# Kernel tuning notes

Measured on AMD Instinct MI355X. Metric: run time of the kernel, lower is better.

The kernel has to match this reference:

```python
import math
import jax, jax.numpy as jnp
import numpy as np

B, T, C, H = 2, 2048, 1024, 16

def setup_inputs() -> dict:
    key = jax.random.key(0)
    k1, k2, k3 = jax.random.split(key, 3)
    x = jax.random.normal(k1, (B, T, C), dtype=jnp.float32)
    W_kqv = jax.random.normal(k2, (C, 3 * C), dtype=jnp.float32) * (1.0 / math.sqrt(C))
    W_proj = jax.random.normal(k3, (C, C), dtype=jnp.float32) * (1.0 / math.sqrt(C))
    b_proj = jnp.zeros((C,), dtype=jnp.float32)
    return {"x": x, "W_kqv": W_kqv, "W_proj": W_proj, "b_proj": b_proj}

def reference(x, W_kqv, W_proj, b_proj):
    Bx, Tx, Cx = x.shape
    hs = Cx // H  # head size
    q, k, v = jnp.split(x @ W_kqv, 3, axis=2)  # each (B,T,C)
    # (B,T,C) -> (B,H,T,hs)
    q = q.reshape(Bx, Tx, H, hs).transpose(0, 2, 1, 3)
    k = k.reshape(Bx, Tx, H, hs).transpose(0, 2, 1, 3)
    v = v.reshape(Bx, Tx, H, hs).transpose(0, 2, 1, 3)
    attn = jnp.einsum('bhqd,bhkd->bhqk', q, k) / math.sqrt(hs)  # (B,H,T,T)
    causal = jnp.tril(jnp.ones((Tx, Tx), dtype=bool))
    attn = jnp.where(causal, attn, -jnp.inf)
    attn = jax.nn.softmax(attn, axis=-1)
    y = jnp.einsum('bhqk,bhkd->bhqd', attn, v)  # (B,H,T,hs)
    y = y.transpose(0, 2, 1, 3).reshape(Bx, Tx, Cx)
    return y @ W_proj + b_proj
```

## Files before the change

### kernel.cpp

```cpp
#include <hip/hip_runtime.h>


typedef unsigned short u16;
typedef unsigned int u32;
typedef __bf16 bf16x8 __attribute__((ext_vector_type(8)));
typedef float f32x4 __attribute__((ext_vector_type(4)));
typedef u32 u32x4 __attribute__((ext_vector_type(4)));
typedef u16 u16x4 __attribute__((ext_vector_type(4)));

__device__ __forceinline__ u16 f2bf(float f) {
  u32 u = __float_as_uint(f);
  u32 r = u + 0x7FFFu + ((u >> 16) & 1u);
  return (u16)(r >> 16);
}

__device__ __forceinline__ bf16x8 ld_bf8(const u16* p) {
  union { u32x4 u; bf16x8 b; } x;
  x.u = *(const u32x4*)p;
  return x.b;
}

__device__ __forceinline__ void gld_lds16(const u16* g, u16* l) {
  __builtin_amdgcn_global_load_lds(
      (const __attribute__((address_space(1))) u32*)g,
      (__attribute__((address_space(3))) u32*)l, 16, 0, 0);
}

__global__ __launch_bounds__(256) void conv_x_kernel(const float* __restrict__ src,
                                                     u16* __restrict__ dst) {
  int idx = blockIdx.x * 256 + threadIdx.x;
  const float4* s4 = (const float4*)src;
  float4 a = s4[2 * idx], b = s4[2 * idx + 1];
  union { u16 h[8]; u32x4 v; } pk;
  pk.h[0] = f2bf(a.x); pk.h[1] = f2bf(a.y); pk.h[2] = f2bf(a.z); pk.h[3] = f2bf(a.w);
  pk.h[4] = f2bf(b.x); pk.h[5] = f2bf(b.y); pk.h[6] = f2bf(b.z); pk.h[7] = f2bf(b.w);
  *(u32x4*)&dst[(size_t)idx * 8] = pk.v;
}

__global__ __launch_bounds__(256) void convT_kernel(const float* __restrict__ src,
                                                    u16* __restrict__ dst, int R, int Cc) {
  __shared__ float ls[64][65];
  int r0 = blockIdx.x * 64, c0 = blockIdx.y * 64;
  int t = threadIdx.x;
  for (int u = t; u < 1024; u += 256) {
    int r = u >> 4, cs = (u & 15) << 2;
    float4 v = *(const float4*)&src[(size_t)(r0 + r) * Cc + (c0 + cs)];
    ls[r][cs] = v.x; ls[r][cs + 1] = v.y; ls[r][cs + 2] = v.z; ls[r][cs + 3] = v.w;
  }
  __syncthreads();
  for (int u = t; u < 1024; u += 256) {
    int n = u >> 4, ks = (u & 15) << 2;
    u16x4 o;
    o.x = f2bf(ls[ks][n]); o.y = f2bf(ls[ks + 1][n]);
    o.z = f2bf(ls[ks + 2][n]); o.w = f2bf(ls[ks + 3][n]);
    *(u16x4*)&dst[(size_t)(c0 + n) * R + (r0 + ks)] = o;
  }
}

__global__ __launch_bounds__(256) void qkv_gemm_kernel(
    const u16* __restrict__ A, const u16* __restrict__ Bt,
    u16* __restrict__ Qh, u16* __restrict__ Kh, u16* __restrict__ Vh, float qscale) {
  constexpr int K = 1024;
  __shared__ __align__(16) u16 As[128 * 32];
  __shared__ __align__(16) u16 Bs[128 * 32];
  int t = threadIdx.x;
  int wave = t >> 6, lane = t & 63, quad = lane >> 4, l16 = lane & 15;
  int wm = (wave >> 1) << 6, wn = (wave & 1) << 6;
  int m0 = blockIdx.x * 128, n0 = blockIdx.y * 128;
  f32x4 acc[4][4] = {};
  int u0 = t, u1 = t + 256;
  int ra0 = u0 >> 2, ca0 = ((u0 & 3) ^ ((u0 >> 3) & 3)) << 3;
  int ra1 = u1 >> 2, ca1 = ((u1 & 3) ^ ((u1 >> 3) & 3)) << 3;
  int swq = (quad ^ ((l16 >> 1) & 3)) << 3;
  for (int k0 = 0; k0 < K; k0 += 32) {
    gld_lds16(&A[(size_t)(m0 + ra0) * K + k0 + ca0], &As[u0 * 8]);
    gld_lds16(&A[(size_t)(m0 + ra1) * K + k0 + ca1], &As[u1 * 8]);
    gld_lds16(&Bt[(size_t)(n0 + ra0) * K + k0 + ca0], &Bs[u0 * 8]);
    gld_lds16(&Bt[(size_t)(n0 + ra1) * K + k0 + ca1], &Bs[u1 * 8]);
    __syncthreads();
    bf16x8 af[4], bfr[4];
    for (int r = 0; r < 4; ++r) af[r] = ld_bf8(&As[(wm + r * 16 + l16) * 32 + swq]);
    for (int c = 0; c < 4; ++c) bfr[c] = ld_bf8(&Bs[(wn + c * 16 + l16) * 32 + swq]);
    for (int r = 0; r < 4; ++r)
      for (int c = 0; c < 4; ++c)
        acc[r][c] = __builtin_amdgcn_mfma_f32_16x16x32_bf16(af[r], bfr[c], acc[r][c], 0, 0, 0);
    __syncthreads();
  }
  for (int r = 0; r < 4; ++r) {
    int rowbase = m0 + wm + r * 16 + quad * 4;
    for (int c = 0; c < 4; ++c) {
      int col = n0 + wn + c * 16 + l16;
      int seg = col >> 10;
      int cc = col & 1023;
      int h = cc >> 6, d = cc & 63;
      for (int i = 0; i < 4; ++i) {
        int row = rowbase + i;
        int b = row >> 11, tt = row & 2047;
        size_t off = (((size_t)(b * 16 + h)) * 2048 + tt) * 64 + d;
        float v = acc[r][c][i];
        if (seg == 0)      Qh[off] = f2bf(v * qscale);
        else if (seg == 1) Kh[off] = f2bf(v);
        else               Vh[off] = f2bf(v);
      }
    }
  }
}

__global__ __launch_bounds__(256) void vT_kernel(const u16* __restrict__ Vh,
                                                 u16* __restrict__ Vt) {
  __shared__ __align__(16) u16 ls[64 * 72];
  int t = threadIdx.x;
  int t0 = blockIdx.x * 64, bh = blockIdx.y;
  const u16* in = Vh + ((size_t)bh * 2048 + t0) * 64;
  for (int u = t; u < 512; u += 256) {
    int row = u >> 3, col = (u & 7) << 3;
    *(u32x4*)&ls[row * 72 + col] = *(const u32x4*)&in[(size_t)row * 64 + col];
  }
  __syncthreads();
  for (int u = t; u < 512; u += 256) {
    int d = u >> 3, tc = (u & 7) << 3;
    union { u16 h[8]; u32x4 v; } pk;
    for (int j = 0; j < 8; ++j) pk.h[j] = ls[(tc + j) * 72 + d];
    *(u32x4*)&Vt[((size_t)bh * 64 + d) * 2048 + t0 + tc] = pk.v;
  }
}

__global__ __launch_bounds__(512) void proj_gemm_kernel(
    const u16* __restrict__ A, const u16* __restrict__ Bt,
    float* __restrict__ out, const float* __restrict__ bias) {
  constexpr int K = 1024;
  __shared__ __align__(16) u16 As[128 * 32];
  __shared__ __align__(16) u16 Bs[128 * 32];
  int t = threadIdx.x;
  int wave = t >> 6, lane = t & 63, quad = lane >> 4, l16 = lane & 15;
  int wm = (wave >> 2) << 6, wn = (wave & 3) << 5;
  int m0 = blockIdx.x * 128, n0 = blockIdx.y * 128;
  f32x4 acc[4][2] = {};
  int u0 = t;
  int ra0 = u0 >> 2, ca0 = ((u0 & 3) ^ ((u0 >> 3) & 3)) << 3;
  int swq = (quad ^ ((l16 >> 1) & 3)) << 3;
  for (int k0 = 0; k0 < K; k0 += 32) {
    gld_lds16(&A[(size_t)(m0 + ra0) * K + k0 + ca0], &As[u0 * 8]);
    gld_lds16(&Bt[(size_t)(n0 + ra0) * K + k0 + ca0], &Bs[u0 * 8]);
    __syncthreads();
    bf16x8 af[4], bfr[2];
    for (int r = 0; r < 4; ++r) af[r] = ld_bf8(&As[(wm + r * 16 + l16) * 32 + swq]);
    for (int c = 0; c < 2; ++c) bfr[c] = ld_bf8(&Bs[(wn + c * 16 + l16) * 32 + swq]);
    for (int r = 0; r < 4; ++r)
      for (int c = 0; c < 2; ++c)
        acc[r][c] = __builtin_amdgcn_mfma_f32_16x16x32_bf16(af[r], bfr[c], acc[r][c], 0, 0, 0);
    __syncthreads();
  }
  for (int r = 0; r < 4; ++r) {
    int rowbase = m0 + wm + r * 16 + quad * 4;
    for (int c = 0; c < 2; ++c) {
      int col = n0 + wn + c * 16 + l16;
      float bv = bias[col];
      for (int i = 0; i < 4; ++i)
        out[(size_t)(rowbase + i) * 1024 + col] = acc[r][c][i] + bv;
    }
  }
}

__global__ __launch_bounds__(256, 6) void flash_kernel(
    const u16* __restrict__ Qh, const u16* __restrict__ Kh, const u16* __restrict__ Vt,
    u16* __restrict__ yb, float* __restrict__ Opart) {
  __shared__ __align__(16) u16 Ks[64 * 64];
  __shared__ __align__(16) u16 Vs[64 * 64];
  __shared__ __align__(16) u16 Ps[64 * 64];
  int t = threadIdx.x, wave = t >> 6, lane = t & 63, quad = lane >> 4, l16 = lane & 15;
  int id = blockIdx.x;
  int g = id / 360, r = id % 360;
  int bh = g * 8 + (r & 7);
  int jx = r >> 3;
  int qtile, kvs, kve, sidx = 0, half = 0;
  bool partial;
  if (jx < 19) {
    qtile = 18 - jx; kvs = 0; kve = qtile + 1; partial = false;
  } else {
    sidx = (jx - 19) >> 1; half = (jx - 19) & 1;
    qtile = 31 - sidx;
    int nkv = qtile + 1, mid = nkv >> 1;
    kvs = half ? mid : 0; kve = half ? nkv : mid; partial = true;
  }
  int q0 = qtile << 6;
  const u16* Qb = Qh + (size_t)bh * 2048 * 64;
  const u16* Kb = Kh + (size_t)bh * 2048 * 64;
  const u16* Vb = Vt + (size_t)bh * 64 * 2048;
  bf16x8 qa0, qa1;
  {
    int qrow = q0 + wave * 16 + l16;
    qa0 = ld_bf8(&Qb[(size_t)qrow * 64 + quad * 8]);
    qa1 = ld_bf8(&Qb[(size_t)qrow * 64 + 32 + quad * 8]);
  }
  f32x4 oacc[4] = {};
  float lsum = 0.f;
  int u0 = wave * 128 + lane, u1 = u0 + 64;
  int r0 = u0 >> 3, p0 = u0 & 7, cb0 = (p0 - r0) & 7;
  int r1s = u1 >> 3, p1 = u1 & 7, cb1 = (p1 - r1s) & 7;
  for (int j = kvs; j < kve; ++j) {
    int kv0 = j << 6;
    __syncthreads();
    gld_lds16(&Kb[(size_t)(kv0 + r0) * 64 + cb0 * 8], &Ks[u0 * 8]);
    gld_lds16(&Kb[(size_t)(kv0 + r1s) * 64 + cb1 * 8], &Ks[u1 * 8]);
    gld_lds16(&Vb[(size_t)r0 * 2048 + kv0 + cb0 * 8], &Vs[u0 * 8]);
    gld_lds16(&Vb[(size_t)r1s * 2048 + kv0 + cb1 * 8], &Vs[u1 * 8]);
    __syncthreads();
    bool maskit = (j == qtile);
    for (int c = 0; c < 4; ++c) {
      int krow = c * 16 + l16;
      bf16x8 kb0 = ld_bf8(&Ks[krow * 64 + ((quad + krow) & 7) * 8]);
      bf16x8 kb1 = ld_bf8(&Ks[krow * 64 + ((quad + 4 + krow) & 7) * 8]);
      f32x4 z = {0.f, 0.f, 0.f, 0.f};
      z = __builtin_amdgcn_mfma_f32_16x16x32_bf16(kb0, qa0, z, 0, 0, 0);
      z = __builtin_amdgcn_mfma_f32_16x16x32_bf16(kb1, qa1, z, 0, 0, 0);
      int prow = wave * 16 + l16;
      union { u16 hh[4]; u16x4 v; } pk;
      for (int i = 0; i < 4; ++i) {
        float p = __builtin_amdgcn_exp2f(z[i]);
        if (maskit && (kv0 + c * 16 + quad * 4 + i > q0 + wave * 16 + l16)) p = 0.f;
        lsum += p;
        pk.hh[i] = f2bf(p);
      }
      *(u16x4*)&Ps[prow * 64 + ((2 * c + (quad >> 1) + prow) & 7) * 8 + (quad & 1) * 4] = pk.v;
    }
    int prow = wave * 16 + l16;
    bf16x8 pa0 = ld_bf8(&Ps[prow * 64 + ((quad + prow) & 7) * 8]);
    bf16x8 pa1 = ld_bf8(&Ps[prow * 64 + ((quad + 4 + prow) & 7) * 8]);
    for (int dt = 0; dt < 4; ++dt) {
      int vrow = dt * 16 + l16;
      bf16x8 vb0 = ld_bf8(&Vs[vrow * 64 + ((quad + vrow) & 7) * 8]);
      bf16x8 vb1 = ld_bf8(&Vs[vrow * 64 + ((quad + 4 + vrow) & 7) * 8]);
      oacc[dt] = __builtin_amdgcn_mfma_f32_16x16x32_bf16(pa0, vb0, oacc[dt], 0, 0, 0);
      oacc[dt] = __builtin_amdgcn_mfma_f32_16x16x32_bf16(pa1, vb1, oacc[dt], 0, 0, 0);
    }
  }
  lsum += __shfl_xor(lsum, 16);
  lsum += __shfl_xor(lsum, 32);
  if (partial) {
    float* Op = Opart + ((size_t)(bh * 13 + sidx) * 2 + half) * 4160;
    for (int dt = 0; dt < 4; ++dt)
      for (int i = 0; i < 4; ++i)
        Op[(wave * 16 + quad * 4 + i) * 64 + dt * 16 + l16] = oacc[dt][i];
    if (quad == 0) Op[4096 + wave * 16 + l16] = lsum;
  } else {
    int b = bh >> 4, h = bh & 15;
    for (int i = 0; i < 4; ++i) {
      float inv = 1.0f / __shfl(lsum, quad * 4 + i);
      int qq = q0 + wave * 16 + quad * 4 + i;
      size_t rowoff = ((size_t)(b * 2048 + qq)) * 1024 + h * 64;
      for (int dt = 0; dt < 4; ++dt)
        yb[rowoff + dt * 16 + l16] = f2bf(oacc[dt][i] * inv);
    }
  }
}

__global__ __launch_bounds__(256) void combine_kernel(const float* __restrict__ Opart,
                                                      u16* __restrict__ yb) {
  int sidx = blockIdx.x, bh = blockIdx.y, t = threadIdx.x;
  int qtile = 31 - sidx;
  const float* A = Opart + (size_t)(bh * 13 + sidx) * 2 * 4160;
  const float* Bp = A + 4160;
  int q = t >> 2, d0 = (t & 3) << 4;
  float inv = 1.0f / (A[4096 + q] + Bp[4096 + q]);
  int b = bh >> 4, h = bh & 15;
  size_t off = ((size_t)(b * 2048 + (qtile << 6) + q)) * 1024 + h * 64 + d0;
  union { u16 hh[16]; u32x4 v[2]; } pk;
  for (int k = 0; k < 16; ++k)
    pk.hh[k] = f2bf((A[q * 64 + d0 + k] + Bp[q * 64 + d0 + k]) * inv);
  *(u32x4*)&yb[off] = pk.v[0];
  *(u32x4*)&yb[off + 8] = pk.v[1];
}

extern "C" void kernel_launch(void* const* d_in, const int* in_sizes, int n_in,
                              void* d_out, int out_size, void* d_ws, size_t ws_size,
                              hipStream_t stream) {
  const float* x     = (const float*)d_in[0];
  const float* Wkqv  = (const float*)d_in[1];
  const float* Wproj = (const float*)d_in[2];
  const float* bproj = (const float*)d_in[3];
  float* out = (float*)d_out;

  u16* ws     = (u16*)d_ws;
  u16* xb     = ws;
  u16* wkqvT  = xb + (size_t)4096 * 1024;
  u16* wprojT = wkqvT + (size_t)3072 * 1024;
  u16* Qh     = wprojT + (size_t)1024 * 1024;
  u16* Kh     = Qh + (size_t)32 * 2048 * 64;
  u16* Vt     = Kh + (size_t)32 * 2048 * 64;
  u16* yb     = Vt + (size_t)32 * 2048 * 64;
  u16* Vh     = yb;
  float* Opart = (float*)ws;

  const float QSCALE = 0.18033688011112042f;

  conv_x_kernel<<<2048, 256, 0, stream>>>(x, xb);
  convT_kernel<<<dim3(16, 48), 256, 0, stream>>>(Wkqv, wkqvT, 1024, 3072);
  convT_kernel<<<dim3(16, 16), 256, 0, stream>>>(Wproj, wprojT, 1024, 1024);
  qkv_gemm_kernel<<<dim3(32, 24), 256, 0, stream>>>(xb, wkqvT, Qh, Kh, Vh, QSCALE);
  vT_kernel<<<dim3(32, 32), 256, 0, stream>>>(Vh, Vt);
  flash_kernel<<<1440, 256, 0, stream>>>(Qh, Kh, Vt, yb, Opart);
  combine_kernel<<<dim3(13, 32), 256, 0, stream>>>(Opart, yb);
  proj_gemm_kernel<<<dim3(32, 8), 512, 0, stream>>>(yb, wprojT, out, bproj);
}
```

Measured before the change: 189.3 us.

## Fuse prep kernels, write V transposed from QKV GEMM, widen flash waves

```diff
diff --git a/kernel.cpp b/kernel.cpp
--- a/kernel.cpp
+++ b/kernel.cpp
@@ -26,43 +26,56 @@
       (__attribute__((address_space(3))) u32*)l, 16, 0, 0);
 }
 
-__global__ __launch_bounds__(256) void conv_x_kernel(const float* __restrict__ src,
-                                                     u16* __restrict__ dst) {
-  int idx = blockIdx.x * 256 + threadIdx.x;
-  const float4* s4 = (const float4*)src;
-  float4 a = s4[2 * idx], b = s4[2 * idx + 1];
-  union { u16 h[8]; u32x4 v; } pk;
-  pk.h[0] = f2bf(a.x); pk.h[1] = f2bf(a.y); pk.h[2] = f2bf(a.z); pk.h[3] = f2bf(a.w);
-  pk.h[4] = f2bf(b.x); pk.h[5] = f2bf(b.y); pk.h[6] = f2bf(b.z); pk.h[7] = f2bf(b.w);
-  *(u32x4*)&dst[(size_t)idx * 8] = pk.v;
-}
-
-__global__ __launch_bounds__(256) void convT_kernel(const float* __restrict__ src,
-                                                    u16* __restrict__ dst, int R, int Cc) {
-  __shared__ float ls[64][65];
-  int r0 = blockIdx.x * 64, c0 = blockIdx.y * 64;
+__device__ __forceinline__ void convT_body(const float* __restrict__ src,
+                                           u16* __restrict__ dst, int R, int Cc,
+                                           int r0, int c0, float* ls ) {
   int t = threadIdx.x;
   for (int u = t; u < 1024; u += 256) {
     int r = u >> 4, cs = (u & 15) << 2;
     float4 v = *(const float4*)&src[(size_t)(r0 + r) * Cc + (c0 + cs)];
-    ls[r][cs] = v.x; ls[r][cs + 1] = v.y; ls[r][cs + 2] = v.z; ls[r][cs + 3] = v.w;
+    ls[r * 65 + cs] = v.x; ls[r * 65 + cs + 1] = v.y;
+    ls[r * 65 + cs + 2] = v.z; ls[r * 65 + cs + 3] = v.w;
   }
   __syncthreads();
   for (int u = t; u < 1024; u += 256) {
     int n = u >> 4, ks = (u & 15) << 2;
     u16x4 o;
-    o.x = f2bf(ls[ks][n]); o.y = f2bf(ls[ks + 1][n]);
-    o.z = f2bf(ls[ks + 2][n]); o.w = f2bf(ls[ks + 3][n]);
+    o.x = f2bf(ls[ks * 65 + n]); o.y = f2bf(ls[(ks + 1) * 65 + n]);
+    o.z = f2bf(ls[(ks + 2) * 65 + n]); o.w = f2bf(ls[(ks + 3) * 65 + n]);
     *(u16x4*)&dst[(size_t)(c0 + n) * R + (r0 + ks)] = o;
+  }
+}
+
+__global__ __launch_bounds__(256) void prep_kernel(
+    const float* __restrict__ x, const float* __restrict__ Wkqv,
+    const float* __restrict__ Wproj, u16* __restrict__ xb,
+    u16* __restrict__ wkqvT, u16* __restrict__ wprojT) {
+  __shared__ float ls[64 * 65];
+  int bx = blockIdx.x;
+  if (bx < 2048) {
+    int idx = bx * 256 + threadIdx.x;
+    const float4* s4 = (const float4*)x;
+    float4 a = s4[2 * idx], b = s4[2 * idx + 1];
+    union { u16 h[8]; u32x4 v; } pk;
+    pk.h[0] = f2bf(a.x); pk.h[1] = f2bf(a.y); pk.h[2] = f2bf(a.z); pk.h[3] = f2bf(a.w);
+    pk.h[4] = f2bf(b.x); pk.h[5] = f2bf(b.y); pk.h[6] = f2bf(b.z); pk.h[7] = f2bf(b.w);
+    *(u32x4*)&xb[(size_t)idx * 8] = pk.v;
+  } else if (bx < 2816) {
+    int idx = bx - 2048;
+    convT_body(Wkqv, wkqvT, 1024, 3072, (idx & 15) * 64, (idx >> 4) * 64, ls);
+  } else {
+    int idx = bx - 2816;
+    convT_body(Wproj, wprojT, 1024, 1024, (idx & 15) * 64, (idx >> 4) * 64, ls);
   }
 }
 
 __global__ __launch_bounds__(256) void qkv_gemm_kernel(
     const u16* __restrict__ A, const u16* __restrict__ Bt,
-    u16* __restrict__ Qh, u16* __restrict__ Kh, u16* __restrict__ Vh, float qscale) {
+    u16* __restrict__ Qh, u16* __restrict__ Kh, u16* __restrict__ Vt, float qscale) {
   constexpr int K = 1024;
-  __shared__ __align__(16) u16 As[128 * 32];
-  __shared__ __align__(16) u16 Bs[128 * 32];
+  __shared__ __align__(16) u16 smem[8704];
+  u16* As = smem;
+  u16* Bs = smem + 4096;
   int t = threadIdx.x;
   int wave = t >> 6, lane = t & 63, quad = lane >> 4, l16 = lane & 15;
   int wm = (wave >> 1) << 6, wn = (wave & 1) << 6;
@@ -86,42 +99,48 @@
         acc[r][c] = __builtin_amdgcn_mfma_f32_16x16x32_bf16(af[r], bfr[c], acc[r][c], 0, 0, 0);
     __syncthreads();
   }
-  for (int r = 0; r < 4; ++r) {
-    int rowbase = m0 + wm + r * 16 + quad * 4;
-    for (int c = 0; c < 4; ++c) {
-      int col = n0 + wn + c * 16 + l16;
-      int seg = col >> 10;
-      int cc = col & 1023;
-      int h = cc >> 6, d = cc & 63;
-      for (int i = 0; i < 4; ++i) {
-        int row = rowbase + i;
-        int b = row >> 11, tt = row & 2047;
-        size_t off = (((size_t)(b * 16 + h)) * 2048 + tt) * 64 + d;
-        float v = acc[r][c][i];
-        if (seg == 0)      Qh[off] = f2bf(v * qscale);
-        else if (seg == 1) Kh[off] = f2bf(v);
-        else               Vh[off] = f2bf(v);
-      }
-    }
-  }
-}
-
-__global__ __launch_bounds__(256) void vT_kernel(const u16* __restrict__ Vh,
-                                                 u16* __restrict__ Vt) {
-  __shared__ __align__(16) u16 ls[64 * 72];
-  int t = threadIdx.x;
-  int t0 = blockIdx.x * 64, bh = blockIdx.y;
-  const u16* in = Vh + ((size_t)bh * 2048 + t0) * 64;
-  for (int u = t; u < 512; u += 256) {
-    int row = u >> 3, col = (u & 7) << 3;
-    *(u32x4*)&ls[row * 72 + col] = *(const u32x4*)&in[(size_t)row * 64 + col];
-  }
-  __syncthreads();
-  for (int u = t; u < 512; u += 256) {
-    int d = u >> 3, tc = (u & 7) << 3;
-    union { u16 h[8]; u32x4 v; } pk;
-    for (int j = 0; j < 8; ++j) pk.h[j] = ls[(tc + j) * 72 + d];
-    *(u32x4*)&Vt[((size_t)bh * 64 + d) * 2048 + t0 + tc] = pk.v;
+  if (n0 < 2048) {
+    for (int r = 0; r < 4; ++r) {
+      int rowbase = m0 + wm + r * 16 + quad * 4;
+      for (int c = 0; c < 4; ++c) {
+        int col = n0 + wn + c * 16 + l16;
+        int seg = col >> 10;
+        int cc = col & 1023;
+        int h = cc >> 6, d = cc & 63;
+        for (int i = 0; i < 4; ++i) {
+          int row = rowbase + i;
+          int b = row >> 11, tt = row & 2047;
+          size_t off = (((size_t)(b * 16 + h)) * 2048 + tt) * 64 + d;
+          float v = acc[r][c][i];
+          if (seg == 0) Qh[off] = f2bf(v * qscale);
+          else          Kh[off] = f2bf(v);
+        }
+      }
+    }
+  } else {
+    int h0 = (n0 - 2048) >> 6;
+    int b = m0 >> 11, tt0 = m0 & 2047;
+    for (int p = 0; p < 2; ++p) {
+      __syncthreads();
+      if (wn == p * 64) {
+        for (int r = 0; r < 4; ++r) {
+          int row = wm + r * 16 + quad * 4;
+          for (int c = 0; c < 4; ++c) {
+            int col = c * 16 + l16;
+            union { u16 hh[4]; u16x4 v; } pk;
+            for (int i = 0; i < 4; ++i) pk.hh[i] = f2bf(acc[r][c][i]);
+            *(u16x4*)&smem[col * 136 + row] = pk.v;
+          }
+        }
+      }
+      __syncthreads();
+      int bh = b * 16 + h0 + p;
+      for (int w = t; w < 1024; w += 256) {
+        int col = w >> 4, ch = w & 15;
+        u32x4 v = *(u32x4*)&smem[col * 136 + ch * 8];
+        *(u32x4*)&Vt[((size_t)bh * 64 + col) * 2048 + tt0 + ch * 8] = v;
+      }
+    }
   }
 }
 
@@ -162,7 +181,7 @@
   }
 }
 
-__global__ __launch_bounds__(256, 6) void flash_kernel(
+__global__ __launch_bounds__(128, 3) void flash_kernel(
     const u16* __restrict__ Qh, const u16* __restrict__ Kh, const u16* __restrict__ Vt,
     u16* __restrict__ yb, float* __restrict__ Opart) {
   __shared__ __align__(16) u16 Ks[64 * 64];
@@ -187,71 +206,92 @@
   const u16* Qb = Qh + (size_t)bh * 2048 * 64;
   const u16* Kb = Kh + (size_t)bh * 2048 * 64;
   const u16* Vb = Vt + (size_t)bh * 64 * 2048;
-  bf16x8 qa0, qa1;
-  {
-    int qrow = q0 + wave * 16 + l16;
-    qa0 = ld_bf8(&Qb[(size_t)qrow * 64 + quad * 8]);
-    qa1 = ld_bf8(&Qb[(size_t)qrow * 64 + 32 + quad * 8]);
-  }
-  f32x4 oacc[4] = {};
-  float lsum = 0.f;
-  int u0 = wave * 128 + lane, u1 = u0 + 64;
-  int r0 = u0 >> 3, p0 = u0 & 7, cb0 = (p0 - r0) & 7;
-  int r1s = u1 >> 3, p1 = u1 & 7, cb1 = (p1 - r1s) & 7;
+  bf16x8 qa[2][2];
+  for (int s = 0; s < 2; ++s) {
+    int qrow = q0 + wave * 32 + s * 16 + l16;
+    qa[s][0] = ld_bf8(&Qb[(size_t)qrow * 64 + quad * 8]);
+    qa[s][1] = ld_bf8(&Qb[(size_t)qrow * 64 + 32 + quad * 8]);
+  }
+  f32x4 oacc[2][4] = {};
+  float lsum[2] = {0.f, 0.f};
   for (int j = kvs; j < kve; ++j) {
     int kv0 = j << 6;
     __syncthreads();
-    gld_lds16(&Kb[(size_t)(kv0 + r0) * 64 + cb0 * 8], &Ks[u0 * 8]);
-    gld_lds16(&Kb[(size_t)(kv0 + r1s) * 64 + cb1 * 8], &Ks[u1 * 8]);
-    gld_lds16(&Vb[(size_t)r0 * 2048 + kv0 + cb0 * 8], &Vs[u0 * 8]);
-    gld_lds16(&Vb[(size_t)r1s * 2048 + kv0 + cb1 * 8], &Vs[u1 * 8]);
+    for (int k = 0; k < 4; ++k) {
+      int u = wave * 256 + k * 64 + lane;
+      int row = u >> 3, cb = ((u & 7) - row) & 7;
+      gld_lds16(&Kb[(size_t)(kv0 + row) * 64 + cb * 8], &Ks[u * 8]);
+      gld_lds16(&Vb[(size_t)row * 2048 + kv0 + cb * 8], &Vs[u * 8]);
+    }
     __syncthreads();
     bool maskit = (j == qtile);
     for (int c = 0; c < 4; ++c) {
       int krow = c * 16 + l16;
       bf16x8 kb0 = ld_bf8(&Ks[krow * 64 + ((quad + krow) & 7) * 8]);
       bf16x8 kb1 = ld_bf8(&Ks[krow * 64 + ((quad + 4 + krow) & 7) * 8]);
-      f32x4 z = {0.f, 0.f, 0.f, 0.f};
-      z = __builtin_amdgcn_mfma_f32_16x16x32_bf16(kb0, qa0, z, 0, 0, 0);
-      z = __builtin_amdgcn_mfma_f32_16x16x32_bf16(kb1, qa1, z, 0, 0, 0);
-      int prow = wave * 16 + l16;
-      union { u16 hh[4]; u16x4 v; } pk;
-      for (int i = 0; i < 4; ++i) {
-        float p = __builtin_amdgcn_exp2f(z[i]);
-        if (maskit && (kv0 + c * 16 + quad * 4 + i > q0 + wave * 16 + l16)) p = 0.f;
-        lsum += p;
-        pk.hh[i] = f2bf(p);
-      }
-      *(u16x4*)&Ps[prow * 64 + ((2 * c + (quad >> 1) + prow) & 7) * 8 + (quad & 1) * 4] = pk.v;
-    }
-    int prow = wave * 16 + l16;
-    bf16x8 pa0 = ld_bf8(&Ps[prow * 64 + ((quad + prow) & 7) * 8]);
-    bf16x8 pa1 = ld_bf8(&Ps[prow * 64 + ((quad + 4 + prow) & 7) * 8]);
+      for (int s = 0; s < 2; ++s) {
+        f32x4 z = {0.f, 0.f, 0.f, 0.f};
+        z = __builtin_amdgcn_mfma_f32_16x16x32_bf16(kb0, qa[s][0], z, 0, 0, 0);
+        z = __builtin_amdgcn_mfma_f32_16x16x32_bf16(kb1, qa[s][1], z, 0, 0, 0);
+        int prow = wave * 32 + s * 16 + l16;
+        union { u16 hh[4]; u16x4 v; } pk;
+        if (maskit) {
+          int qg = q0 + prow;
+          for (int i = 0; i < 4; ++i) {
+            float p = __builtin_amdgcn_exp2f(z[i]);
+            if (kv0 + c * 16 + quad * 4 + i > qg) p = 0.f;
+            lsum[s] += p;
+            pk.hh[i] = f2bf(p);
+          }
+        } else {
+          for (int i = 0; i < 4; ++i) {
+            float p = __builtin_amdgcn_exp2f(z[i]);
+            lsum[s] += p;
+            pk.hh[i] = f2bf(p);
+          }
+        }
+        *(u16x4*)&Ps[prow * 64 + ((2 * c + (quad >> 1) + prow) & 7) * 8 + (quad & 1) * 4] =
+            pk.v;
+      }
+    }
+    bf16x8 pa[2][2];
+    for (int s = 0; s < 2; ++s) {
+      int prow = wave * 32 + s * 16 + l16;
+      pa[s][0] = ld_bf8(&Ps[prow * 64 + ((quad + prow) & 7) * 8]);
+      pa[s][1] = ld_bf8(&Ps[prow * 64 + ((quad + 4 + prow) & 7) * 8]);
+    }
     for (int dt = 0; dt < 4; ++dt) {
       int vrow = dt * 16 + l16;
       bf16x8 vb0 = ld_bf8(&Vs[vrow * 64 + ((quad + vrow) & 7) * 8]);
       bf16x8 vb1 = ld_bf8(&Vs[vrow * 64 + ((quad + 4 + vrow) & 7) * 8]);
-      oacc[dt] = __builtin_amdgcn_mfma_f32_16x16x32_bf16(pa0, vb0, oacc[dt], 0, 0, 0);
-      oacc[dt] = __builtin_amdgcn_mfma_f32_16x16x32_bf16(pa1, vb1, oacc[dt], 0, 0, 0);
-    }
-  }
-  lsum += __shfl_xor(lsum, 16);
-  lsum += __shfl_xor(lsum, 32);
+      for (int s = 0; s < 2; ++s) {
+        oacc[s][dt] = __builtin_amdgcn_mfma_f32_16x16x32_bf16(pa[s][0], vb0, oacc[s][dt], 0, 0, 0);
+        oacc[s][dt] = __builtin_amdgcn_mfma_f32_16x16x32_bf16(pa[s][1], vb1, oacc[s][dt], 0, 0, 0);
+      }
+    }
+  }
+  for (int s = 0; s < 2; ++s) {
+    lsum[s] += __shfl_xor(lsum[s], 16);
+    lsum[s] += __shfl_xor(lsum[s], 32);
+  }
   if (partial) {
     float* Op = Opart + ((size_t)(bh * 13 + sidx) * 2 + half) * 4160;
-    for (int dt = 0; dt < 4; ++dt)
-      for (int i = 0; i < 4; ++i)
-        Op[(wave * 16 + quad * 4 + i) * 64 + dt * 16 + l16] = oacc[dt][i];
-    if (quad == 0) Op[4096 + wave * 16 + l16] = lsum;
+    for (int s = 0; s < 2; ++s) {
+      for (int dt = 0; dt < 4; ++dt)
+        for (int i = 0; i < 4; ++i)
+          Op[(wave * 32 + s * 16 + quad * 4 + i) * 64 + dt * 16 + l16] = oacc[s][dt][i];
+      if (quad == 0) Op[4096 + wave * 32 + s * 16 + l16] = lsum[s];
+    }
   } else {
     int b = bh >> 4, h = bh & 15;
-    for (int i = 0; i < 4; ++i) {
-      float inv = 1.0f / __shfl(lsum, quad * 4 + i);
-      int qq = q0 + wave * 16 + quad * 4 + i;
-      size_t rowoff = ((size_t)(b * 2048 + qq)) * 1024 + h * 64;
-      for (int dt = 0; dt < 4; ++dt)
-        yb[rowoff + dt * 16 + l16] = f2bf(oacc[dt][i] * inv);
-    }
+    for (int s = 0; s < 2; ++s)
+      for (int i = 0; i < 4; ++i) {
+        float inv = 1.0f / __shfl(lsum[s], quad * 4 + i);
+        int qq = q0 + wave * 32 + s * 16 + quad * 4 + i;
+        size_t rowoff = ((size_t)(b * 2048 + qq)) * 1024 + h * 64;
+        for (int dt = 0; dt < 4; ++dt)
+          yb[rowoff + dt * 16 + l16] = f2bf(oacc[s][dt][i] * inv);
+      }
   }
 }
 
@@ -289,17 +329,13 @@
   u16* Kh     = Qh + (size_t)32 * 2048 * 64;
   u16* Vt     = Kh + (size_t)32 * 2048 * 64;
   u16* yb     = Vt + (size_t)32 * 2048 * 64;
-  u16* Vh     = yb;
   float* Opart = (float*)ws;
 
   const float QSCALE = 0.18033688011112042f;
 
-  conv_x_kernel<<<2048, 256, 0, stream>>>(x, xb);
-  convT_kernel<<<dim3(16, 48), 256, 0, stream>>>(Wkqv, wkqvT, 1024, 3072);
-  convT_kernel<<<dim3(16, 16), 256, 0, stream>>>(Wproj, wprojT, 1024, 1024);
-  qkv_gemm_kernel<<<dim3(32, 24), 256, 0, stream>>>(xb, wkqvT, Qh, Kh, Vh, QSCALE);
-  vT_kernel<<<dim3(32, 32), 256, 0, stream>>>(Vh, Vt);
-  flash_kernel<<<1440, 256, 0, stream>>>(Qh, Kh, Vt, yb, Opart);
+  prep_kernel<<<3072, 256, 0, stream>>>(x, Wkqv, Wproj, xb, wkqvT, wprojT);
+  qkv_gemm_kernel<<<dim3(32, 24), 256, 0, stream>>>(xb, wkqvT, Qh, Kh, Vt, QSCALE);
+  flash_kernel<<<1440, 128, 0, stream>>>(Qh, Kh, Vt, yb, Opart);
   combine_kernel<<<dim3(13, 32), 256, 0, stream>>>(Opart, yb);
   proj_gemm_kernel<<<dim3(32, 8), 512, 0, stream>>>(yb, wprojT, out, bproj);
 }
```

After: 205.0 us. +8.3%, slower.

## Fuse prep conversions into one launch, retile proj GEMM, split masked softmax path

Applied to the files above, without the earlier changes.

```diff
diff --git a/kernel.cpp b/kernel.cpp
--- a/kernel.cpp
+++ b/kernel.cpp
@@ -26,34 +26,46 @@
       (__attribute__((address_space(3))) u32*)l, 16, 0, 0);
 }
 
-__global__ __launch_bounds__(256) void conv_x_kernel(const float* __restrict__ src,
-                                                     u16* __restrict__ dst) {
-  int idx = blockIdx.x * 256 + threadIdx.x;
-  const float4* s4 = (const float4*)src;
-  float4 a = s4[2 * idx], b = s4[2 * idx + 1];
-  union { u16 h[8]; u32x4 v; } pk;
-  pk.h[0] = f2bf(a.x); pk.h[1] = f2bf(a.y); pk.h[2] = f2bf(a.z); pk.h[3] = f2bf(a.w);
-  pk.h[4] = f2bf(b.x); pk.h[5] = f2bf(b.y); pk.h[6] = f2bf(b.z); pk.h[7] = f2bf(b.w);
-  *(u32x4*)&dst[(size_t)idx * 8] = pk.v;
-}
-
-__global__ __launch_bounds__(256) void convT_kernel(const float* __restrict__ src,
-                                                    u16* __restrict__ dst, int R, int Cc) {
-  __shared__ float ls[64][65];
-  int r0 = blockIdx.x * 64, c0 = blockIdx.y * 64;
+__device__ __forceinline__ void convT_body(const float* __restrict__ src,
+                                           u16* __restrict__ dst, int R, int Cc,
+                                           int r0, int c0, float* ls ) {
   int t = threadIdx.x;
   for (int u = t; u < 1024; u += 256) {
     int r = u >> 4, cs = (u & 15) << 2;
     float4 v = *(const float4*)&src[(size_t)(r0 + r) * Cc + (c0 + cs)];
-    ls[r][cs] = v.x; ls[r][cs + 1] = v.y; ls[r][cs + 2] = v.z; ls[r][cs + 3] = v.w;
+    ls[r * 65 + cs] = v.x; ls[r * 65 + cs + 1] = v.y;
+    ls[r * 65 + cs + 2] = v.z; ls[r * 65 + cs + 3] = v.w;
   }
   __syncthreads();
   for (int u = t; u < 1024; u += 256) {
     int n = u >> 4, ks = (u & 15) << 2;
     u16x4 o;
-    o.x = f2bf(ls[ks][n]); o.y = f2bf(ls[ks + 1][n]);
-    o.z = f2bf(ls[ks + 2][n]); o.w = f2bf(ls[ks + 3][n]);
+    o.x = f2bf(ls[ks * 65 + n]); o.y = f2bf(ls[(ks + 1) * 65 + n]);
+    o.z = f2bf(ls[(ks + 2) * 65 + n]); o.w = f2bf(ls[(ks + 3) * 65 + n]);
     *(u16x4*)&dst[(size_t)(c0 + n) * R + (r0 + ks)] = o;
+  }
+}
+
+__global__ __launch_bounds__(256) void prep_kernel(
+    const float* __restrict__ x, const float* __restrict__ Wkqv,
+    const float* __restrict__ Wproj, u16* __restrict__ xb,
+    u16* __restrict__ wkqvT, u16* __restrict__ wprojT) {
+  __shared__ float ls[64 * 65];
+  int bx = blockIdx.x;
+  if (bx < 2048) {
+    int idx = bx * 256 + threadIdx.x;
+    const float4* s4 = (const float4*)x;
+    float4 a = s4[2 * idx], b = s4[2 * idx + 1];
+    union { u16 h[8]; u32x4 v; } pk;
+    pk.h[0] = f2bf(a.x); pk.h[1] = f2bf(a.y); pk.h[2] = f2bf(a.z); pk.h[3] = f2bf(a.w);
+    pk.h[4] = f2bf(b.x); pk.h[5] = f2bf(b.y); pk.h[6] = f2bf(b.z); pk.h[7] = f2bf(b.w);
+    *(u32x4*)&xb[(size_t)idx * 8] = pk.v;
+  } else if (bx < 2816) {
+    int idx = bx - 2048;
+    convT_body(Wkqv, wkqvT, 1024, 3072, (idx & 15) * 64, (idx >> 4) * 64, ls);
+  } else {
+    int idx = bx - 2816;
+    convT_body(Wproj, wprojT, 1024, 1024, (idx & 15) * 64, (idx >> 4) * 64, ls);
   }
 }
 
@@ -125,17 +137,17 @@
   }
 }
 
-__global__ __launch_bounds__(512) void proj_gemm_kernel(
+__global__ __launch_bounds__(256) void proj_gemm_kernel(
     const u16* __restrict__ A, const u16* __restrict__ Bt,
     float* __restrict__ out, const float* __restrict__ bias) {
   constexpr int K = 1024;
-  __shared__ __align__(16) u16 As[128 * 32];
-  __shared__ __align__(16) u16 Bs[128 * 32];
+  __shared__ __align__(16) u16 As[64 * 32];
+  __shared__ __align__(16) u16 Bs[64 * 32];
   int t = threadIdx.x;
   int wave = t >> 6, lane = t & 63, quad = lane >> 4, l16 = lane & 15;
-  int wm = (wave >> 2) << 6, wn = (wave & 3) << 5;
-  int m0 = blockIdx.x * 128, n0 = blockIdx.y * 128;
-  f32x4 acc[4][2] = {};
+  int wm = (wave >> 1) << 5, wn = (wave & 1) << 5;
+  int m0 = blockIdx.x * 64, n0 = blockIdx.y * 64;
+  f32x4 acc[2][2] = {};
   int u0 = t;
   int ra0 = u0 >> 2, ca0 = ((u0 & 3) ^ ((u0 >> 3) & 3)) << 3;
   int swq = (quad ^ ((l16 >> 1) & 3)) << 3;
@@ -143,15 +155,15 @@
     gld_lds16(&A[(size_t)(m0 + ra0) * K + k0 + ca0], &As[u0 * 8]);
     gld_lds16(&Bt[(size_t)(n0 + ra0) * K + k0 + ca0], &Bs[u0 * 8]);
     __syncthreads();
-    bf16x8 af[4], bfr[2];
-    for (int r = 0; r < 4; ++r) af[r] = ld_bf8(&As[(wm + r * 16 + l16) * 32 + swq]);
+    bf16x8 af[2], bfr[2];
+    for (int r = 0; r < 2; ++r) af[r] = ld_bf8(&As[(wm + r * 16 + l16) * 32 + swq]);
     for (int c = 0; c < 2; ++c) bfr[c] = ld_bf8(&Bs[(wn + c * 16 + l16) * 32 + swq]);
-    for (int r = 0; r < 4; ++r)
+    for (int r = 0; r < 2; ++r)
       for (int c = 0; c < 2; ++c)
         acc[r][c] = __builtin_amdgcn_mfma_f32_16x16x32_bf16(af[r], bfr[c], acc[r][c], 0, 0, 0);
     __syncthreads();
   }
-  for (int r = 0; r < 4; ++r) {
+  for (int r = 0; r < 2; ++r) {
     int rowbase = m0 + wm + r * 16 + quad * 4;
     for (int c = 0; c < 2; ++c) {
       int col = n0 + wn + c * 16 + l16;
@@ -216,11 +228,20 @@
       z = __builtin_amdgcn_mfma_f32_16x16x32_bf16(kb1, qa1, z, 0, 0, 0);
       int prow = wave * 16 + l16;
       union { u16 hh[4]; u16x4 v; } pk;
-      for (int i = 0; i < 4; ++i) {
-        float p = __builtin_amdgcn_exp2f(z[i]);
-        if (maskit && (kv0 + c * 16 + quad * 4 + i > q0 + wave * 16 + l16)) p = 0.f;
-        lsum += p;
-        pk.hh[i] = f2bf(p);
+      if (maskit) {
+        int qg = q0 + prow;
+        for (int i = 0; i < 4; ++i) {
+          float p = __builtin_amdgcn_exp2f(z[i]);
+          if (kv0 + c * 16 + quad * 4 + i > qg) p = 0.f;
+          lsum += p;
+          pk.hh[i] = f2bf(p);
+        }
+      } else {
+        for (int i = 0; i < 4; ++i) {
+          float p = __builtin_amdgcn_exp2f(z[i]);
+          lsum += p;
+          pk.hh[i] = f2bf(p);
+        }
       }
       *(u16x4*)&Ps[prow * 64 + ((2 * c + (quad >> 1) + prow) & 7) * 8 + (quad & 1) * 4] = pk.v;
     }
@@ -294,12 +315,10 @@
 
   const float QSCALE = 0.18033688011112042f;
 
-  conv_x_kernel<<<2048, 256, 0, stream>>>(x, xb);
-  convT_kernel<<<dim3(16, 48), 256, 0, stream>>>(Wkqv, wkqvT, 1024, 3072);
-  convT_kernel<<<dim3(16, 16), 256, 0, stream>>>(Wproj, wprojT, 1024, 1024);
+  prep_kernel<<<3072, 256, 0, stream>>>(x, Wkqv, Wproj, xb, wkqvT, wprojT);
   qkv_gemm_kernel<<<dim3(32, 24), 256, 0, stream>>>(xb, wkqvT, Qh, Kh, Vh, QSCALE);
   vT_kernel<<<dim3(32, 32), 256, 0, stream>>>(Vh, Vt);
   flash_kernel<<<1440, 256, 0, stream>>>(Qh, Kh, Vt, yb, Opart);
   combine_kernel<<<dim3(13, 32), 256, 0, stream>>>(Opart, yb);
-  proj_gemm_kernel<<<dim3(32, 8), 512, 0, stream>>>(yb, wprojT, out, bproj);
-}
+  proj_gemm_kernel<<<dim3(64, 16), 256, 0, stream>>>(yb, wprojT, out, bproj);
+}
```

Measured after the change: 180.3 us. -4.8%, faster.
